# Performance work log

Hardware: AMD Instinct MI355X
Metric: run time of the kernel (lower is better)

Reference implementation:

```python
import jax, jax.numpy as jnp
import numpy as np

# fHOG orientation lookup (cos/sin of k*20 degrees), exactly the hardcoded
# constants used in Felzenszwalb's features.cc / mmcv extract_hog kernel.
UU = jnp.array([1.0000, 0.9397, 0.7660, 0.5000, 0.1736,
                -0.1736, -0.5000, -0.7660, -0.9397], dtype=jnp.float32)
VV = jnp.array([0.0000, 0.3420, 0.6428, 0.8660, 0.9848,
                0.9848, 0.8660, 0.6428, 0.3420], dtype=jnp.float32)
EPS = 1e-4


def _hog(img, sbin):
    B, C, H, W = img.shape
    bh = int(round(H / sbin)); bw = int(round(W / sbin))
    vh, vw = bh * sbin, bw * sbin
    # central differences at pixels (1..visible-2), source index clamped to dim-2
    ys = jnp.clip(jnp.arange(1, vh - 1), 0, H - 2)
    xs = jnp.clip(jnp.arange(1, vw - 1), 0, W - 2)
    dy = img[:, :, ys + 1][:, :, :, xs] - img[:, :, ys - 1][:, :, :, xs]
    dx = img[:, :, ys][:, :, :, xs + 1] - img[:, :, ys][:, :, :, xs - 1]
    v = dx * dx + dy * dy                      # [B,3,hg,wg]
    ch = jnp.argmax(v, axis=1, keepdims=True)  # channel with max gradient energy
    dxs = jnp.take_along_axis(dx, ch, axis=1)[:, 0]
    dys = jnp.take_along_axis(dy, ch, axis=1)[:, 0]
    mag = jnp.sqrt(dxs * dxs + dys * dys)      # [B,hg,wg]
    # snap to one of 18 signed orientations
    dot = UU[None, :, None, None] * dxs[:, None] + VV[None, :, None, None] * dys[:, None]
    best_o = jnp.argmax(jnp.concatenate([dot, -dot], axis=1), axis=1)  # [B,hg,wg]
    # bilinear spatial soft-binning into sbin x sbin cells
    yp = (jnp.arange(1, vh - 1, dtype=img.dtype) + 0.5) / sbin - 0.5
    xp = (jnp.arange(1, vw - 1, dtype=img.dtype) + 0.5) / sbin - 0.5
    iyp = jnp.floor(yp).astype(jnp.int32); ixp = jnp.floor(xp).astype(jnp.int32)
    vy0 = yp - iyp; vx0 = xp - ixp; vy1 = 1.0 - vy0; vx1 = 1.0 - vx0
    hg, wg = vh - 2, vw - 2
    bidx = jnp.arange(B)[:, None, None]
    IY = jnp.broadcast_to(iyp[None, :, None], (B, hg, wg))
    IX = jnp.broadcast_to(ixp[None, None, :], (B, hg, wg))
    WY0 = vy0[None, :, None]; WY1 = vy1[None, :, None]
    WX0 = vx0[None, None, :]; WX1 = vx1[None, None, :]
    hist = jnp.zeros((B, 18, bh, bw), dtype=img.dtype)

    def scat(h, iy, ix, w):
        valid = (iy >= 0) & (iy < bh) & (ix >= 0) & (ix < bw)
        iyc = jnp.clip(iy, 0, bh - 1); ixc = jnp.clip(ix, 0, bw - 1)
        return h.at[bidx, best_o, iyc, ixc].add(jnp.where(valid, w * mag, 0.0))

    hist = scat(hist, IY, IX, WY1 * WX1)
    hist = scat(hist, IY, IX + 1, WY1 * WX0)
    hist = scat(hist, IY + 1, IX, WY0 * WX1)
    hist = scat(hist, IY + 1, IX + 1, WY0 * WX0)
    # cell energy from contrast-insensitive sums
    s = hist[:, :9] + hist[:, 9:]
    norm = jnp.sum(s * s, axis=1)              # [B,bh,bw]
    # 2x2 block sums of norm
    T = norm[:, :-1, :-1] + norm[:, 1:, :-1] + norm[:, :-1, 1:] + norm[:, 1:, 1:]
    n1 = jax.lax.rsqrt(T[:, 1:, 1:] + EPS)[:, None]
    n2 = jax.lax.rsqrt(T[:, :-1, 1:] + EPS)[:, None]
    n3 = jax.lax.rsqrt(T[:, 1:, :-1] + EPS)[:, None]
    n4 = jax.lax.rsqrt(T[:, :-1, :-1] + EPS)[:, None]
    src = hist[:, :, 1:-1, 1:-1]               # [B,18,oh,ow]
    h1 = jnp.minimum(src * n1, 0.2); h2 = jnp.minimum(src * n2, 0.2)
    h3 = jnp.minimum(src * n3, 0.2); h4 = jnp.minimum(src * n4, 0.2)
    f_cs = 0.5 * (h1 + h2 + h3 + h4)           # 18 contrast-sensitive feats
    ss = src[:, :9] + src[:, 9:]
    f_ci = 0.5 * (jnp.minimum(ss * n1, 0.2) + jnp.minimum(ss * n2, 0.2)
                  + jnp.minimum(ss * n3, 0.2) + jnp.minimum(ss * n4, 0.2))
    tex = 0.2357 * jnp.stack([h1.sum(1), h2.sum(1), h3.sum(1), h4.sum(1)], axis=1)
    feat = jnp.concatenate([f_cs, f_ci, tex], axis=1)  # [B,31,oh,ow]
    return jnp.pad(feat, ((0, 0), (0, 0), (1, 1), (1, 1)))


def setup_inputs() -> dict:
    key = jax.random.key(0)
    img = jax.random.uniform(key, (16, 3, 512, 512), dtype=jnp.float32)
    return {"input": img, "sbin": 4}


def reference(input, sbin):
    return _hog(input, sbin)
```

## Files before the change

### kernel.cpp

```cpp
#include <hip/hip_runtime.h>

#define BATCH 16
#define H 512
#define W 512
#define BH 128
#define BW 128
#define HG 510
#define WG 510
#define PKW 512


__global__ __launch_bounds__(256) void hog_grad(const float* __restrict__ img,
                                                unsigned int* __restrict__ pk)
{
    int tx = threadIdx.x;
    int gx = blockIdx.x * 64 + tx;
    int y  = blockIdx.y * 4 + threadIdx.y;
    int b  = blockIdx.z;
    if (y >= HG) return;
    int x0 = gx * 4;
    int py = y + 1;
    bool edge = (x0 < 508);

    const float* im = img + (size_t)b * 3 * H * W;

    float bv[4] = {-1.f, -1.f, -1.f, -1.f};
    float bx[4] = {0, 0, 0, 0};
    float by[4] = {0, 0, 0, 0};

#pragma unroll
    for (int c = 0; c < 3; c++) {
        const float* base = im + (size_t)c * H * W;
        const float* ru = base + (size_t)(py - 1) * W;
        const float* rc = base + (size_t)py * W;
        const float* rd = base + (size_t)(py + 1) * W;
        float4 u4 = *(const float4*)(ru + x0);
        float4 c4 = *(const float4*)(rc + x0);
        float2 c2 = *(const float2*)(rc + x0 + 4);
        float4 d4 = *(const float4*)(rd + x0);
        float  us = edge ? ru[x0 + 4] : 0.0f;
        float  ds = edge ? rd[x0 + 4] : 0.0f;

        float dx0 = __fsub_rn(c4.z, c4.x), dx1 = __fsub_rn(c4.w, c4.y);
        float dx2 = __fsub_rn(c2.x, c4.z), dx3 = __fsub_rn(c2.y, c4.w);
        float dy0 = __fsub_rn(d4.y, u4.y), dy1 = __fsub_rn(d4.z, u4.z);
        float dy2 = __fsub_rn(d4.w, u4.w), dy3 = __fsub_rn(ds, us);

        float dxs[4] = {dx0, dx1, dx2, dx3};
        float dys[4] = {dy0, dy1, dy2, dy3};
#pragma unroll
        for (int i = 0; i < 4; i++) {
            float v = __fadd_rn(__fmul_rn(dxs[i], dxs[i]), __fmul_rn(dys[i], dys[i]));
            if (v > bv[i]) { bv[i] = v; bx[i] = dxs[i]; by[i] = dys[i]; }
        }
    }

    const float uu[9] = {1.0f, 0.9397f, 0.766f, 0.5f, 0.1736f, -0.1736f, -0.5f, -0.766f, -0.9397f};
    const float vv[9] = {0.0f, 0.342f, 0.6428f, 0.866f, 0.9848f, 0.9848f, 0.866f, 0.6428f, 0.342f};

    unsigned int pkv[4];
#pragma unroll
    for (int i = 0; i < 4; i++) {
        float mg = __fsqrt_rn(bv[i]);
        float d[9];
#pragma unroll
        for (int o = 0; o < 9; o++)
            d[o] = __fadd_rn(__fmul_rn(uu[o], bx[i]), __fmul_rn(vv[o], by[i]));
        float best = -1e30f; int bo = 0;
#pragma unroll
        for (int o = 0; o < 9; o++) { if (d[o] > best) { best = d[o]; bo = o; } }
#pragma unroll
        for (int o = 0; o < 9; o++) { float nd = -d[o]; if (nd > best) { best = nd; bo = o + 9; } }
        unsigned int v = (__float_as_uint(mg) & 0xFFFFFFE0u) | (unsigned int)bo;
        pkv[i] = (x0 + i < WG) ? v : 0u;
    }
    uint4 o4 = make_uint4(pkv[0], pkv[1], pkv[2], pkv[3]);
    *(uint4*)(pk + ((size_t)b * HG + y) * PKW + x0) = o4;
}

__global__ __launch_bounds__(256) void hog_hist(const unsigned int* __restrict__ pk,
                                                float* __restrict__ hist,
                                                float* __restrict__ nrm)
{
    __shared__ float hl0[18 * 256];
    __shared__ float hl1[18 * 256];
    int cx = threadIdx.x;
    int cy = blockIdx.y * 2 + threadIdx.y;
    int b = blockIdx.z;
    int t = threadIdx.y * 128 + cx;

#pragma unroll
    for (int o = 0; o < 18; o++) { hl0[o * 256 + t] = 0.0f; hl1[o * 256 + t] = 0.0f; }

    const float wt[8] = {0.125f, 0.375f, 0.625f, 0.875f, 0.875f, 0.625f, 0.375f, 0.125f};
    const float wl[4] = {0.0f, 0.125f, 0.375f, 0.625f};
    const float wm[4] = {0.875f, 0.875f, 0.625f, 0.375f};

    const unsigned int* pb = pk + (size_t)b * HG * PKW;
    int ry0 = 4 * cy - 3;
    int xb = 4 * cx;

#pragma unroll
    for (int ky = 0; ky < 8; ky++) {
        int ry = ry0 + ky;
        if ((unsigned)ry >= (unsigned)HG) continue;
        float wy = wt[ky];
        const unsigned int* row = pb + (size_t)ry * PKW;
        if (cx > 0) {
            uint4 L = *(const uint4*)(row + xb - 4);
            { unsigned p = L.y; hl0[(p & 31u) * 256 + t] += (wy * wl[1]) * __uint_as_float(p & 0xFFFFFFE0u); }
            { unsigned p = L.z; hl1[(p & 31u) * 256 + t] += (wy * wl[2]) * __uint_as_float(p & 0xFFFFFFE0u); }
            { unsigned p = L.w; hl0[(p & 31u) * 256 + t] += (wy * wl[3]) * __uint_as_float(p & 0xFFFFFFE0u); }
        }
        uint4 M = *(const uint4*)(row + xb);
        { unsigned p = M.x; hl1[(p & 31u) * 256 + t] += (wy * wm[0]) * __uint_as_float(p & 0xFFFFFFE0u); }
        { unsigned p = M.y; hl0[(p & 31u) * 256 + t] += (wy * wm[1]) * __uint_as_float(p & 0xFFFFFFE0u); }
        if (cx < 127) {
            { unsigned p = M.z; hl1[(p & 31u) * 256 + t] += (wy * wm[2]) * __uint_as_float(p & 0xFFFFFFE0u); }
            { unsigned p = M.w; hl0[(p & 31u) * 256 + t] += (wy * wm[3]) * __uint_as_float(p & 0xFFFFFFE0u); }
            unsigned p = row[xb + 4];
            hl1[(p & 31u) * 256 + t] += (wy * 0.125f) * __uint_as_float(p & 0xFFFFFFE0u);
        }
    }

    float h[18];
#pragma unroll
    for (int o = 0; o < 18; o++) {
        h[o] = hl0[o * 256 + t] + hl1[o * 256 + t];
        hist[(((size_t)b * 18 + o) * BH + cy) * BW + cx] = h[o];
    }
    float s = 0.0f;
#pragma unroll
    for (int o = 0; o < 9; o++) { float ss = h[o] + h[o + 9]; s += ss * ss; }
    nrm[((size_t)b * BH + cy) * BW + cx] = s;
}

__global__ __launch_bounds__(256) void hog_feat(const float* __restrict__ hist,
                                                const float* __restrict__ nrm,
                                                float* __restrict__ out)
{
    int ox = threadIdx.x;
    int oy = blockIdx.y * 2 + threadIdx.y;
    int b = blockIdx.z;

    if (ox == 0 || ox == BW - 1 || oy == 0 || oy == BH - 1) {
#pragma unroll
        for (int c = 0; c < 31; c++)
            out[(((size_t)b * 31 + c) * BH + oy) * BW + ox] = 0.0f;
        return;
    }

    const float* nb = nrm + (size_t)b * BH * BW;
    float n00 = nb[(size_t)(oy - 1) * BW + ox - 1], n01 = nb[(size_t)(oy - 1) * BW + ox], n02 = nb[(size_t)(oy - 1) * BW + ox + 1];
    float n10 = nb[(size_t)oy * BW + ox - 1],       n11 = nb[(size_t)oy * BW + ox],       n12 = nb[(size_t)oy * BW + ox + 1];
    float n20 = nb[(size_t)(oy + 1) * BW + ox - 1], n21 = nb[(size_t)(oy + 1) * BW + ox], n22 = nb[(size_t)(oy + 1) * BW + ox + 1];

    float T11 = n11 + n21 + n12 + n22;
    float T01 = n01 + n11 + n02 + n12;
    float T10 = n10 + n20 + n11 + n21;
    float T00 = n00 + n10 + n01 + n11;
    float v1 = 1.0f / __fsqrt_rn(T11 + 1e-4f);
    float v2 = 1.0f / __fsqrt_rn(T01 + 1e-4f);
    float v3 = 1.0f / __fsqrt_rn(T10 + 1e-4f);
    float v4 = 1.0f / __fsqrt_rn(T00 + 1e-4f);

    float h[18];
#pragma unroll
    for (int o = 0; o < 18; o++)
        h[o] = hist[(((size_t)b * 18 + o) * BH + oy) * BW + ox];

    float t1 = 0.f, t2 = 0.f, t3 = 0.f, t4 = 0.f;
#pragma unroll
    for (int o = 0; o < 18; o++) {
        float s = h[o];
        float a1 = fminf(s * v1, 0.2f);
        float a2 = fminf(s * v2, 0.2f);
        float a3 = fminf(s * v3, 0.2f);
        float a4 = fminf(s * v4, 0.2f);
        out[(((size_t)b * 31 + o) * BH + oy) * BW + ox] = 0.5f * (a1 + a2 + a3 + a4);
        t1 += a1; t2 += a2; t3 += a3; t4 += a4;
    }
#pragma unroll
    for (int o = 0; o < 9; o++) {
        float ss = h[o] + h[o + 9];
        float a1 = fminf(ss * v1, 0.2f);
        float a2 = fminf(ss * v2, 0.2f);
        float a3 = fminf(ss * v3, 0.2f);
        float a4 = fminf(ss * v4, 0.2f);
        out[(((size_t)b * 31 + 18 + o) * BH + oy) * BW + ox] = 0.5f * (a1 + a2 + a3 + a4);
    }
    out[(((size_t)b * 31 + 27) * BH + oy) * BW + ox] = 0.2357f * t1;
    out[(((size_t)b * 31 + 28) * BH + oy) * BW + ox] = 0.2357f * t2;
    out[(((size_t)b * 31 + 29) * BH + oy) * BW + ox] = 0.2357f * t3;
    out[(((size_t)b * 31 + 30) * BH + oy) * BW + ox] = 0.2357f * t4;
}

extern "C" void kernel_launch(void* const* d_in, const int* in_sizes, int n_in,
                              void* d_out, int out_size, void* d_ws, size_t ws_size,
                              hipStream_t stream)
{
    const float* img = (const float*)d_in[0];
    float* out = (float*)d_out;
    char* ws = (char*)d_ws;

    unsigned int* pk = (unsigned int*)ws;
    float* hist      = (float*)(ws + 16715776);
    float* nrm       = (float*)(ws + 35590144);

    dim3 b1(64, 4, 1), g1(2, 128, BATCH);
    hog_grad<<<g1, b1, 0, stream>>>(img, pk);

    dim3 b2(128, 2, 1), g2(1, BH / 2, BATCH);
    hog_hist<<<g2, b2, 0, stream>>>(pk, hist, nrm);
    hog_feat<<<g2, b2, 0, stream>>>(hist, nrm, out);
}
```

Before: 119.3 us.

## Compute 4x4 gradient tile per thread and store histogram as fp16 pairs

```diff
diff --git a/kernel.cpp b/kernel.cpp
--- a/kernel.cpp
+++ b/kernel.cpp
@@ -1,4 +1,5 @@
 #include <hip/hip_runtime.h>
+#include <hip/hip_fp16.h>
 
 #define BATCH 16
 #define H 512
@@ -13,73 +14,83 @@
 __global__ __launch_bounds__(256) void hog_grad(const float* __restrict__ img,
                                                 unsigned int* __restrict__ pk)
 {
-    int tx = threadIdx.x;
-    int gx = blockIdx.x * 64 + tx;
-    int y  = blockIdx.y * 4 + threadIdx.y;
+    int gx = blockIdx.x * 64 + threadIdx.x;
+    int qy = blockIdx.y * 4 + threadIdx.y;
     int b  = blockIdx.z;
-    if (y >= HG) return;
     int x0 = gx * 4;
-    int py = y + 1;
+    int y0 = qy * 4;
     bool edge = (x0 < 508);
 
     const float* im = img + (size_t)b * 3 * H * W;
 
-    float bv[4] = {-1.f, -1.f, -1.f, -1.f};
-    float bx[4] = {0, 0, 0, 0};
-    float by[4] = {0, 0, 0, 0};
+    float bv[16], bx[16], by[16];
+#pragma unroll
+    for (int i = 0; i < 16; i++) { bv[i] = -1.f; bx[i] = 0.f; by[i] = 0.f; }
 
 #pragma unroll
     for (int c = 0; c < 3; c++) {
         const float* base = im + (size_t)c * H * W;
-        const float* ru = base + (size_t)(py - 1) * W;
-        const float* rc = base + (size_t)py * W;
-        const float* rd = base + (size_t)(py + 1) * W;
-        float4 u4 = *(const float4*)(ru + x0);
-        float4 c4 = *(const float4*)(rc + x0);
-        float2 c2 = *(const float2*)(rc + x0 + 4);
-        float4 d4 = *(const float4*)(rd + x0);
-        float  us = edge ? ru[x0 + 4] : 0.0f;
-        float  ds = edge ? rd[x0 + 4] : 0.0f;
-
-        float dx0 = __fsub_rn(c4.z, c4.x), dx1 = __fsub_rn(c4.w, c4.y);
-        float dx2 = __fsub_rn(c2.x, c4.z), dx3 = __fsub_rn(c2.y, c4.w);
-        float dy0 = __fsub_rn(d4.y, u4.y), dy1 = __fsub_rn(d4.z, u4.z);
-        float dy2 = __fsub_rn(d4.w, u4.w), dy3 = __fsub_rn(ds, us);
-
-        float dxs[4] = {dx0, dx1, dx2, dx3};
-        float dys[4] = {dy0, dy1, dy2, dy3};
-#pragma unroll
-        for (int i = 0; i < 4; i++) {
-            float v = __fadd_rn(__fmul_rn(dxs[i], dxs[i]), __fmul_rn(dys[i], dys[i]));
-            if (v > bv[i]) { bv[i] = v; bx[i] = dxs[i]; by[i] = dys[i]; }
+        float Wr[6][6];
+#pragma unroll
+        for (int j = 0; j < 6; j++) {
+            int pr = y0 + j; if (pr > 511) pr = 511;
+            const float* rowp = base + (size_t)pr * W + x0;
+            float4 a = *(const float4*)rowp;
+            Wr[j][0] = a.x; Wr[j][1] = a.y; Wr[j][2] = a.z; Wr[j][3] = a.w;
+            if (j >= 1 && j <= 4) {
+                if (edge || pr < 511) {
+                    float2 f = *(const float2*)(rowp + 4);
+                    Wr[j][4] = f.x; Wr[j][5] = f.y;
+                } else { Wr[j][4] = 0.f; Wr[j][5] = 0.f; }
+            } else {
+                Wr[j][4] = edge ? rowp[4] : 0.0f;
+                Wr[j][5] = 0.f;
+            }
+        }
+#pragma unroll
+        for (int r = 0; r < 4; r++) {
+#pragma unroll
+            for (int i = 0; i < 4; i++) {
+                float dx = __fsub_rn(Wr[r + 1][i + 2], Wr[r + 1][i]);
+                float dy = __fsub_rn(Wr[r + 2][i + 1], Wr[r][i + 1]);
+                float v = __fadd_rn(__fmul_rn(dx, dx), __fmul_rn(dy, dy));
+                int k = r * 4 + i;
+                if (v > bv[k]) { bv[k] = v; bx[k] = dx; by[k] = dy; }
+            }
         }
     }
 
     const float uu[9] = {1.0f, 0.9397f, 0.766f, 0.5f, 0.1736f, -0.1736f, -0.5f, -0.766f, -0.9397f};
     const float vv[9] = {0.0f, 0.342f, 0.6428f, 0.866f, 0.9848f, 0.9848f, 0.866f, 0.6428f, 0.342f};
 
-    unsigned int pkv[4];
-#pragma unroll
-    for (int i = 0; i < 4; i++) {
-        float mg = __fsqrt_rn(bv[i]);
-        float d[9];
-#pragma unroll
-        for (int o = 0; o < 9; o++)
-            d[o] = __fadd_rn(__fmul_rn(uu[o], bx[i]), __fmul_rn(vv[o], by[i]));
-        float best = -1e30f; int bo = 0;
-#pragma unroll
-        for (int o = 0; o < 9; o++) { if (d[o] > best) { best = d[o]; bo = o; } }
-#pragma unroll
-        for (int o = 0; o < 9; o++) { float nd = -d[o]; if (nd > best) { best = nd; bo = o + 9; } }
-        unsigned int v = (__float_as_uint(mg) & 0xFFFFFFE0u) | (unsigned int)bo;
-        pkv[i] = (x0 + i < WG) ? v : 0u;
-    }
-    uint4 o4 = make_uint4(pkv[0], pkv[1], pkv[2], pkv[3]);
-    *(uint4*)(pk + ((size_t)b * HG + y) * PKW + x0) = o4;
+#pragma unroll
+    for (int r = 0; r < 4; r++) {
+        int y = y0 + r;
+        if (y >= HG) break;
+        unsigned int pkv[4];
+#pragma unroll
+        for (int i = 0; i < 4; i++) {
+            int k = r * 4 + i;
+            float mg = __fsqrt_rn(bv[k]);
+            float d[9];
+#pragma unroll
+            for (int o = 0; o < 9; o++)
+                d[o] = __fadd_rn(__fmul_rn(uu[o], bx[k]), __fmul_rn(vv[o], by[k]));
+            float best = -1e30f; int bo = 0;
+#pragma unroll
+            for (int o = 0; o < 9; o++) { if (d[o] > best) { best = d[o]; bo = o; } }
+#pragma unroll
+            for (int o = 0; o < 9; o++) { float nd = -d[o]; if (nd > best) { best = nd; bo = o + 9; } }
+            unsigned int v = (__float_as_uint(mg) & 0xFFFFFFE0u) | (unsigned int)bo;
+            pkv[i] = (x0 + i < WG) ? v : 0u;
+        }
+        uint4 o4 = make_uint4(pkv[0], pkv[1], pkv[2], pkv[3]);
+        *(uint4*)(pk + ((size_t)b * HG + y) * PKW + x0) = o4;
+    }
 }
 
 __global__ __launch_bounds__(256) void hog_hist(const unsigned int* __restrict__ pk,
-                                                float* __restrict__ hist,
+                                                __half2* __restrict__ hist,
                                                 float* __restrict__ nrm)
 {
     __shared__ float hl0[18 * 256];
@@ -123,19 +134,19 @@
         }
     }
 
-    float h[18];
-#pragma unroll
-    for (int o = 0; o < 18; o++) {
-        h[o] = hl0[o * 256 + t] + hl1[o * 256 + t];
-        hist[(((size_t)b * 18 + o) * BH + cy) * BW + cx] = h[o];
-    }
     float s = 0.0f;
 #pragma unroll
-    for (int o = 0; o < 9; o++) { float ss = h[o] + h[o + 9]; s += ss * ss; }
+    for (int o = 0; o < 9; o++) {
+        float lo = hl0[o * 256 + t] + hl1[o * 256 + t];
+        float hi = hl0[(o + 9) * 256 + t] + hl1[(o + 9) * 256 + t];
+        hist[(((size_t)b * 9 + o) * BH + cy) * BW + cx] = __floats2half2_rn(lo, hi);
+        float ss = lo + hi;
+        s += ss * ss;
+    }
     nrm[((size_t)b * BH + cy) * BW + cx] = s;
 }
 
-__global__ __launch_bounds__(256) void hog_feat(const float* __restrict__ hist,
+__global__ __launch_bounds__(256) void hog_feat(const __half2* __restrict__ hist,
                                                 const float* __restrict__ nrm,
                                                 float* __restrict__ out)
 {
@@ -166,8 +177,10 @@
 
     float h[18];
 #pragma unroll
-    for (int o = 0; o < 18; o++)
-        h[o] = hist[(((size_t)b * 18 + o) * BH + oy) * BW + ox];
+    for (int o = 0; o < 9; o++) {
+        float2 f = __half22float2(hist[(((size_t)b * 9 + o) * BH + oy) * BW + ox]);
+        h[o] = f.x; h[o + 9] = f.y;
+    }
 
     float t1 = 0.f, t2 = 0.f, t3 = 0.f, t4 = 0.f;
 #pragma unroll
@@ -204,10 +217,10 @@
     char* ws = (char*)d_ws;
 
     unsigned int* pk = (unsigned int*)ws;
-    float* hist      = (float*)(ws + 16715776);
-    float* nrm       = (float*)(ws + 35590144);
-
-    dim3 b1(64, 4, 1), g1(2, 128, BATCH);
+    __half2* hist    = (__half2*)(ws + 16715776);
+    float* nrm       = (float*)(ws + 26152960);
+
+    dim3 b1(64, 4, 1), g1(2, 32, BATCH);
     hog_grad<<<g1, b1, 0, stream>>>(img, pk);
 
     dim3 b2(128, 2, 1), g2(1, BH / 2, BATCH);
```

After: 118.8 us. Within noise of the previous version (-0.4%).
